# Kernel optimization log

Hardware: AMD Instinct MI355X
Metric: run time of the kernel (lower is better)

The kernel has to match this reference:

```python
import jax, jax.numpy as jnp
import numpy as np

N_NODES = 50000
IN_CH = 128
HID_CH = 128   # 2 * out_channels
OUT_CH = 64
N_EDGES = 800000


def setup_inputs() -> dict:
    key = jax.random.key(0)
    k1, k2, k3, k4 = jax.random.split(key, 4)
    x = jax.random.normal(k1, (N_NODES, IN_CH), dtype=jnp.float32)
    edge_index = jax.random.randint(k2, (2, N_EDGES), 0, N_NODES, dtype=jnp.int64)
    # Glorot-ish init for weights
    W1 = jax.random.normal(k3, (IN_CH, HID_CH), dtype=jnp.float32) * (1.0 / np.sqrt(IN_CH))
    b1 = jnp.zeros((HID_CH,), dtype=jnp.float32)
    W2 = jax.random.normal(k4, (HID_CH, OUT_CH), dtype=jnp.float32) * (1.0 / np.sqrt(HID_CH))
    b2 = jnp.zeros((OUT_CH,), dtype=jnp.float32)
    return {"x": x, "edge_index": edge_index, "W1": W1, "b1": b1, "W2": W2, "b2": b2}


def _gcn_norm(edge_index, num_nodes):
    """Add self-loops and compute symmetric normalization coeffs (PyG GCNConv default)."""
    loops = jnp.arange(num_nodes, dtype=edge_index.dtype)
    src = jnp.concatenate([edge_index[0], loops])  # [E + N]
    dst = jnp.concatenate([edge_index[1], loops])
    ones = jnp.ones_like(dst, dtype=jnp.float32)
    deg = jax.ops.segment_sum(ones, dst, num_segments=num_nodes)  # in-degree incl self-loop
    dinv = jnp.where(deg > 0, jax.lax.rsqrt(deg), 0.0)
    norm = dinv[src] * dinv[dst]  # [E + N]
    return src, dst, norm


def _gcn_conv(x, src, dst, norm, W, b, num_nodes):
    h = x @ W                                        # dense transform [N, d_out]
    msg = h[src] * norm[:, None]                     # gather + scale  [E+N, d_out]
    out = jax.ops.segment_sum(msg, dst, num_segments=num_nodes)  # scatter-add
    return out + b


def reference(x, edge_index, W1, b1, W2, b2):
    n = x.shape[0]
    src, dst, norm = _gcn_norm(edge_index, n)
    h = _gcn_conv(x, src, dst, norm, W1, b1, n)
    h = jax.nn.relu(h)
    out = _gcn_conv(h, src, dst, norm, W2, b2, n)
    return out
```

## Files before the change

### kernel.cpp

```cpp
#include <hip/hip_runtime.h>
#include <hip/hip_fp16.h>
#include <math.h>

#define IN_CH 128
#define CAP 64


__global__ __launch_bounds__(256, 4) void k_gemm_build(
    const float* __restrict__ x, const float* __restrict__ W1,
    __half* __restrict__ g1, int N,
    const int* __restrict__ src, const int* __restrict__ dst,
    int* __restrict__ deg, unsigned short* __restrict__ slot, int E, int GB) {
    constexpr int KC = 32;
    constexpr int AP = KC + 4;
    constexpr int NOUT = 128;
    constexpr int TCG = NOUT / 8;
    constexpr int BST = KC * 8 + 4;
    constexpr int TM = 4;
    __shared__ float As[64 * AP];
    __shared__ float Bs[TCG * BST];
    int tid = threadIdx.x;

    if ((int)blockIdx.x >= GB) {
        int base = ((int)blockIdx.x - GB) * 1024 + tid;
        int es[4], ed[4], er[4];
        bool ev[4];
#pragma unroll
        for (int k = 0; k < 4; ++k) {
            int e = base + k * 256;
            ev[k] = (e < E);
            ed[k] = ev[k] ? dst[e] : 0;
            es[k] = ev[k] ? src[e] : 0;
        }
#pragma unroll
        for (int k = 0; k < 4; ++k) er[k] = ev[k] ? atomicAdd(&deg[ed[k]], 1) : CAP;
#pragma unroll
        for (int k = 0; k < 4; ++k) {
            if (er[k] < CAP) slot[(size_t)ed[k] * CAP + er[k]] = (unsigned short)es[k];
        }
        return;
    }

    int row0 = (int)blockIdx.x * 64;
    int cg = tid % TCG;
    int rg = tid / TCG;
    int r0 = rg * TM;

    float acc[TM][8];
#pragma unroll
    for (int r = 0; r < TM; ++r)
#pragma unroll
        for (int c = 0; c < 8; ++c) acc[r][c] = 0.f;

    for (int kc0 = 0; kc0 < IN_CH; kc0 += KC) {
        if (kc0 > 0) __syncthreads();
        for (int idx = tid; idx < 64 * (KC / 4); idx += 256) {
            int r = idx >> 3;
            int c4 = (idx & 7) * 4;
            float4 v = make_float4(0.f, 0.f, 0.f, 0.f);
            if (row0 + r < N) v = *(const float4*)(x + (size_t)(row0 + r) * IN_CH + kc0 + c4);
            *(float4*)(As + r * AP + c4) = v;
        }
        for (int idx = tid; idx < KC * (NOUT / 4); idx += 256) {
            int kk = idx / (NOUT / 4);
            int col = (idx % (NOUT / 4)) * 4;
            int cgw = col >> 3;
            int j = col & 7;
            *(float4*)(Bs + cgw * BST + kk * 8 + j) = *(const float4*)(W1 + (size_t)(kc0 + kk) * NOUT + col);
        }
        __syncthreads();

        for (int k = 0; k < KC; k += 4) {
            float4 a4[TM];
#pragma unroll
            for (int r = 0; r < TM; ++r) a4[r] = *(const float4*)(As + (r0 + r) * AP + k);
#pragma unroll
            for (int kk = 0; kk < 4; ++kk) {
                float4 b0 = *(const float4*)(Bs + cg * BST + (k + kk) * 8);
                float4 b1 = *(const float4*)(Bs + cg * BST + (k + kk) * 8 + 4);
#pragma unroll
                for (int r = 0; r < TM; ++r) {
                    float a = (kk == 0) ? a4[r].x : (kk == 1) ? a4[r].y : (kk == 2) ? a4[r].z : a4[r].w;
                    acc[r][0] += a * b0.x;
                    acc[r][1] += a * b0.y;
                    acc[r][2] += a * b0.z;
                    acc[r][3] += a * b0.w;
                    acc[r][4] += a * b1.x;
                    acc[r][5] += a * b1.y;
                    acc[r][6] += a * b1.z;
                    acc[r][7] += a * b1.w;
                }
            }
        }
    }

#pragma unroll
    for (int r = 0; r < TM; ++r) {
        int row = row0 + r0 + r;
        if (row < N) {
            union { __half2 h[4]; uint4 u; } cv;
            cv.h[0] = __floats2half2_rn(acc[r][0], acc[r][1]);
            cv.h[1] = __floats2half2_rn(acc[r][2], acc[r][3]);
            cv.h[2] = __floats2half2_rn(acc[r][4], acc[r][5]);
            cv.h[3] = __floats2half2_rn(acc[r][6], acc[r][7]);
            *(uint4*)(g1 + (size_t)row * NOUT + cg * 8) = cv.u;
        }
    }
}

__global__ __launch_bounds__(256) void k_dinv(
    const int* __restrict__ deg, float* __restrict__ dinv, int N) {
    int i = blockIdx.x * 256 + threadIdx.x;
    if (i < N) dinv[i] = rsqrtf((float)(deg[i] + 1));
}


__global__ __launch_bounds__(256, 4) void k_gemm64(
    const __half* __restrict__ A, const float* __restrict__ W,
    const float* __restrict__ dinv, __half* __restrict__ G, int M) {
    constexpr int KC = 32;
    constexpr int AP = KC + 4;
    constexpr int NOUT = 64;
    constexpr int TCG = NOUT / 8;
    constexpr int BST = KC * 8 + 4;
    constexpr int TM = 2;
    __shared__ float As[64 * AP];
    __shared__ float Bs[TCG * BST];
    int tid = threadIdx.x;
    int row0 = blockIdx.x * 64;
    int cg = tid % TCG;
    int rg = tid / TCG;
    int r0 = rg * TM;

    float acc[TM][8];
#pragma unroll
    for (int r = 0; r < TM; ++r)
#pragma unroll
        for (int c = 0; c < 8; ++c) acc[r][c] = 0.f;

    for (int kc0 = 0; kc0 < IN_CH; kc0 += KC) {
        if (kc0 > 0) __syncthreads();
        {
            int r = tid >> 2;
            int grp = tid & 3;
            float f[8];
            if (row0 + r < M) {
                uint4 raw = *(const uint4*)(A + (size_t)(row0 + r) * IN_CH + kc0 + grp * 8);
                const __half2* h2 = (const __half2*)&raw;
#pragma unroll
                for (int q = 0; q < 4; ++q) {
                    float2 fv = __half22float2(h2[q]);
                    f[2 * q] = fv.x;
                    f[2 * q + 1] = fv.y;
                }
            } else {
#pragma unroll
                for (int q = 0; q < 8; ++q) f[q] = 0.f;
            }
            *(float4*)(As + r * AP + grp * 8) = make_float4(f[0], f[1], f[2], f[3]);
            *(float4*)(As + r * AP + grp * 8 + 4) = make_float4(f[4], f[5], f[6], f[7]);
        }
        for (int idx = tid; idx < KC * (NOUT / 4); idx += 256) {
            int kk = idx / (NOUT / 4);
            int col = (idx % (NOUT / 4)) * 4;
            int cgw = col >> 3;
            int j = col & 7;
            *(float4*)(Bs + cgw * BST + kk * 8 + j) = *(const float4*)(W + (size_t)(kc0 + kk) * NOUT + col);
        }
        __syncthreads();

        for (int k = 0; k < KC; k += 4) {
            float4 a4[TM];
#pragma unroll
            for (int r = 0; r < TM; ++r) a4[r] = *(const float4*)(As + (r0 + r) * AP + k);
#pragma unroll
            for (int kk = 0; kk < 4; ++kk) {
                float4 b0 = *(const float4*)(Bs + cg * BST + (k + kk) * 8);
                float4 b1 = *(const float4*)(Bs + cg * BST + (k + kk) * 8 + 4);
#pragma unroll
                for (int r = 0; r < TM; ++r) {
                    float a = (kk == 0) ? a4[r].x : (kk == 1) ? a4[r].y : (kk == 2) ? a4[r].z : a4[r].w;
                    acc[r][0] += a * b0.x;
                    acc[r][1] += a * b0.y;
                    acc[r][2] += a * b0.z;
                    acc[r][3] += a * b0.w;
                    acc[r][4] += a * b1.x;
                    acc[r][5] += a * b1.y;
                    acc[r][6] += a * b1.z;
                    acc[r][7] += a * b1.w;
                }
            }
        }
    }

#pragma unroll
    for (int r = 0; r < TM; ++r) {
        int row = row0 + r0 + r;
        if (row < M) {
            float d = dinv[row];
            union { __half2 h[4]; uint4 u; } cv;
            cv.h[0] = __floats2half2_rn(d * acc[r][0], d * acc[r][1]);
            cv.h[1] = __floats2half2_rn(d * acc[r][2], d * acc[r][3]);
            cv.h[2] = __floats2half2_rn(d * acc[r][4], d * acc[r][5]);
            cv.h[3] = __floats2half2_rn(d * acc[r][6], d * acc[r][7]);
            *(uint4*)(G + (size_t)row * NOUT + cg * 8) = cv.u;
        }
    }
}


__global__ __launch_bounds__(256) void k_agg128(
    const __half* __restrict__ g, const float* __restrict__ dinv,
    const unsigned short* __restrict__ slot,
    const float* __restrict__ bias, __half* __restrict__ out, int N,
    const int* __restrict__ deg) {
    int wave = threadIdx.x >> 6, lane = threadIdx.x & 63;
    int i = blockIdx.x * 4 + wave;
    if (i >= N) return;
    const __half2* gp = (const __half2*)g;
    int m = min(deg[i], CAP);
    float dinv_i = dinv[i];
    float2 self = __half22float2(gp[(size_t)i * 64 + lane]);
    float2 acc = make_float2(dinv_i * self.x, dinv_i * self.y);
    const unsigned short* sl = slot + (size_t)i * CAP;
    int r = 0;
    for (; r + 8 <= m; r += 8) {
        uint4 sraw = *(const uint4*)(sl + r);
        const unsigned short* sv = (const unsigned short*)&sraw;
        int s[8];
#pragma unroll
        for (int j = 0; j < 8; ++j) s[j] = sv[j];
        __half2 v[8];
#pragma unroll
        for (int j = 0; j < 8; ++j) v[j] = gp[(size_t)s[j] * 64 + lane];
        float ds[8];
#pragma unroll
        for (int j = 0; j < 8; ++j) ds[j] = dinv[s[j]];
#pragma unroll
        for (int j = 0; j < 8; ++j) {
            float2 f = __half22float2(v[j]);
            acc.x += ds[j] * f.x;
            acc.y += ds[j] * f.y;
        }
    }
    for (; r < m; ++r) {
        int s = sl[r];
        float dsv = dinv[s];
        float2 f = __half22float2(gp[(size_t)s * 64 + lane]);
        acc.x += dsv * f.x;
        acc.y += dsv * f.y;
    }
    float2 b = ((const float2*)bias)[lane];
    float ox = fmaxf(dinv_i * acc.x + b.x, 0.f);
    float oy = fmaxf(dinv_i * acc.y + b.y, 0.f);
    ((__half2*)out)[(size_t)i * 64 + lane] = __floats2half2_rn(ox, oy);
}

__global__ __launch_bounds__(256) void k_agg64(
    const __half* __restrict__ g, const float* __restrict__ dinv,
    const unsigned short* __restrict__ slot,
    const float* __restrict__ bias, float* __restrict__ out, int N,
    const int* __restrict__ deg) {
    int wave = threadIdx.x >> 6, lane = threadIdx.x & 63;
    int i = blockIdx.x * 4 + wave;
    if (i >= N) return;
    int m = min(deg[i], CAP);
    float dinv_i = dinv[i];
    float acc = __half2float(g[(size_t)i * 64 + lane]);
    const unsigned short* sl = slot + (size_t)i * CAP;
    int r = 0;
    for (; r + 8 <= m; r += 8) {
        uint4 sraw = *(const uint4*)(sl + r);
        const unsigned short* sv = (const unsigned short*)&sraw;
        int s[8];
#pragma unroll
        for (int j = 0; j < 8; ++j) s[j] = sv[j];
        __half v[8];
#pragma unroll
        for (int j = 0; j < 8; ++j) v[j] = g[(size_t)s[j] * 64 + lane];
#pragma unroll
        for (int j = 0; j < 8; ++j) acc += __half2float(v[j]);
    }
    for (; r < m; ++r) acc += __half2float(g[(size_t)sl[r] * 64 + lane]);
    out[(size_t)i * 64 + lane] = dinv_i * acc + bias[lane];
}


static inline size_t align256(size_t x) { return (x + 255) & ~(size_t)255; }

extern "C" void kernel_launch(void* const* d_in, const int* in_sizes, int n_in,
                              void* d_out, int out_size, void* d_ws, size_t ws_size,
                              hipStream_t stream) {
    const float* x = (const float*)d_in[0];
    const int* ei = (const int*)d_in[1];
    const float* W1 = (const float*)d_in[2];
    const float* b1 = (const float*)d_in[3];
    const float* W2 = (const float*)d_in[4];
    const float* b2 = (const float*)d_in[5];
    float* out = (float*)d_out;

    const int N = in_sizes[0] / IN_CH;
    const int E = in_sizes[1] / 2;
    const int* src = ei;
    const int* dst = ei + E;

    char* p = (char*)d_ws;
    int* deg = (int*)p;                 p += align256((size_t)N * 4);
    float* dinv = (float*)p;            p += align256((size_t)N * 4);
    unsigned short* slot = (unsigned short*)p;  p += align256((size_t)N * CAP * 2);
    __half* g1 = (__half*)p;            p += align256((size_t)N * 128 * 2);
    __half* a1 = (__half*)p;            p += align256((size_t)N * 128 * 2);
    __half* g2 = g1;

    const int GB = (N + 63) / 64;
    const int BB = (E + 1023) / 1024;

    hipMemsetAsync(deg, 0, (size_t)N * 4, stream);
    k_gemm_build<<<GB + BB, 256, 0, stream>>>(x, W1, g1, N, src, dst, deg, slot, E, GB);
    k_dinv<<<(N + 255) / 256, 256, 0, stream>>>(deg, dinv, N);
    k_agg128<<<(N + 3) / 4, 256, 0, stream>>>(g1, dinv, slot, b1, a1, N, deg);
    k_gemm64<<<GB, 256, 0, stream>>>(a1, W2, dinv, g2, N);
    k_agg64<<<(N + 3) / 4, 256, 0, stream>>>(g2, dinv, slot, b2, out, N, deg);
}
```

Baseline: 222.6 us.

## Fuse layer-1 aggregation into layer-2 GEMM via shared-memory tile

The first-layer neighbor aggregation (with bias and ReLU) is merged into the second-layer GEMM kernel. Each block aggregates its 64 rows into a float tile in shared memory, then multiplies that tile by W2. This removes the round trip of the fp16 a1 intermediate through global memory and one kernel launch, and adds a 16-wide unrolled gather loop. In exchange, only 782 blocks (4 waves each, 16 rows per wave, done in sequence) do the latency-bound gather, with more shared memory per block, so the memory parallelism available to hide gather latency may drop.

```diff
diff --git a/kernel.cpp b/kernel.cpp
--- a/kernel.cpp
+++ b/kernel.cpp
@@ -114,20 +114,91 @@
     if (i < N) dinv[i] = rsqrtf((float)(deg[i] + 1));
 }
 
-
-__global__ __launch_bounds__(256, 4) void k_gemm64(
-    const __half* __restrict__ A, const float* __restrict__ W,
-    const float* __restrict__ dinv, __half* __restrict__ G, int M) {
+__global__ __launch_bounds__(256, 3) void k_agg_gemm64(
+    const __half* __restrict__ g, const float* __restrict__ dinv,
+    const unsigned short* __restrict__ slot, const int* __restrict__ deg,
+    const float* __restrict__ b1, const float* __restrict__ W2,
+    __half* __restrict__ G, int N) {
+    constexpr int AFS = 132;
     constexpr int KC = 32;
-    constexpr int AP = KC + 4;
     constexpr int NOUT = 64;
     constexpr int TCG = NOUT / 8;
     constexpr int BST = KC * 8 + 4;
     constexpr int TM = 2;
-    __shared__ float As[64 * AP];
+    __shared__ float Af[64 * AFS];
     __shared__ float Bs[TCG * BST];
     int tid = threadIdx.x;
-    int row0 = blockIdx.x * 64;
+    int wave = tid >> 6, lane = tid & 63;
+    int row0 = (int)blockIdx.x * 64;
+    const __half2* gp = (const __half2*)g;
+
+    for (int t = 0; t < 16; ++t) {
+        int il = wave * 16 + t;
+        int i = row0 + il;
+        float2 acc = make_float2(0.f, 0.f);
+        if (i < N) {
+            int m = min(deg[i], CAP);
+            float di = dinv[i];
+            float2 self = __half22float2(gp[(size_t)i * 64 + lane]);
+            acc.x = di * self.x;
+            acc.y = di * self.y;
+            const unsigned short* sl = slot + (size_t)i * CAP;
+            int r = 0;
+            for (; r + 16 <= m; r += 16) {
+                uint4 sr0 = *(const uint4*)(sl + r);
+                uint4 sr1 = *(const uint4*)(sl + r + 8);
+                const unsigned short* sv0 = (const unsigned short*)&sr0;
+                const unsigned short* sv1 = (const unsigned short*)&sr1;
+                int s[16];
+#pragma unroll
+                for (int j = 0; j < 8; ++j) { s[j] = sv0[j]; s[8 + j] = sv1[j]; }
+                __half2 v[16];
+#pragma unroll
+                for (int j = 0; j < 16; ++j) v[j] = gp[(size_t)s[j] * 64 + lane];
+                float ds[16];
+#pragma unroll
+                for (int j = 0; j < 16; ++j) ds[j] = dinv[s[j]];
+#pragma unroll
+                for (int j = 0; j < 16; ++j) {
+                    float2 f = __half22float2(v[j]);
+                    acc.x += ds[j] * f.x;
+                    acc.y += ds[j] * f.y;
+                }
+            }
+            for (; r + 8 <= m; r += 8) {
+                uint4 sraw = *(const uint4*)(sl + r);
+                const unsigned short* sv = (const unsigned short*)&sraw;
+                int s[8];
+#pragma unroll
+                for (int j = 0; j < 8; ++j) s[j] = sv[j];
+                __half2 v[8];
+#pragma unroll
+                for (int j = 0; j < 8; ++j) v[j] = gp[(size_t)s[j] * 64 + lane];
+                float ds[8];
+#pragma unroll
+                for (int j = 0; j < 8; ++j) ds[j] = dinv[s[j]];
+#pragma unroll
+                for (int j = 0; j < 8; ++j) {
+                    float2 f = __half22float2(v[j]);
+                    acc.x += ds[j] * f.x;
+                    acc.y += ds[j] * f.y;
+                }
+            }
+            for (; r < m; ++r) {
+                int s = sl[r];
+                float dsv = dinv[s];
+                float2 f = __half22float2(gp[(size_t)s * 64 + lane]);
+                acc.x += dsv * f.x;
+                acc.y += dsv * f.y;
+            }
+            float2 b = ((const float2*)b1)[lane];
+            acc.x = fmaxf(di * acc.x + b.x, 0.f);
+            acc.y = fmaxf(di * acc.y + b.y, 0.f);
+        }
+        *(float2*)(Af + il * AFS + 2 * lane) = acc;
+    }
+    __syncthreads();
+
     int cg = tid % TCG;
     int rg = tid / TCG;
     int r0 = rg * TM;
@@ -140,43 +211,23 @@
 
     for (int kc0 = 0; kc0 < IN_CH; kc0 += KC) {
         if (kc0 > 0) __syncthreads();
-        {
-            int r = tid >> 2;
-            int grp = tid & 3;
-            float f[8];
-            if (row0 + r < M) {
-                uint4 raw = *(const uint4*)(A + (size_t)(row0 + r) * IN_CH + kc0 + grp * 8);
-                const __half2* h2 = (const __half2*)&raw;
-#pragma unroll
-                for (int q = 0; q < 4; ++q) {
-                    float2 fv = __half22float2(h2[q]);
-                    f[2 * q] = fv.x;
-                    f[2 * q + 1] = fv.y;
-                }
-            } else {
-#pragma unroll
-                for (int q = 0; q < 8; ++q) f[q] = 0.f;
-            }
-            *(float4*)(As + r * AP + grp * 8) = make_float4(f[0], f[1], f[2], f[3]);
-            *(float4*)(As + r * AP + grp * 8 + 4) = make_float4(f[4], f[5], f[6], f[7]);
-        }
         for (int idx = tid; idx < KC * (NOUT / 4); idx += 256) {
             int kk = idx / (NOUT / 4);
             int col = (idx % (NOUT / 4)) * 4;
             int cgw = col >> 3;
             int j = col & 7;
-            *(float4*)(Bs + cgw * BST + kk * 8 + j) = *(const float4*)(W + (size_t)(kc0 + kk) * NOUT + col);
+            *(float4*)(Bs + cgw * BST + kk * 8 + j) = *(const float4*)(W2 + (size_t)(kc0 + kk) * NOUT + col);
         }
         __syncthreads();
 
         for (int k = 0; k < KC; k += 4) {
             float4 a4[TM];
 #pragma unroll
-            for (int r = 0; r < TM; ++r) a4[r] = *(const float4*)(As + (r0 + r) * AP + k);
+            for (int r = 0; r < TM; ++r) a4[r] = *(const float4*)(Af + (r0 + r) * AFS + kc0 + k);
 #pragma unroll
             for (int kk = 0; kk < 4; ++kk) {
                 float4 b0 = *(const float4*)(Bs + cg * BST + (k + kk) * 8);
-                float4 b1 = *(const float4*)(Bs + cg * BST + (k + kk) * 8 + 4);
+                float4 b1v = *(const float4*)(Bs + cg * BST + (k + kk) * 8 + 4);
 #pragma unroll
                 for (int r = 0; r < TM; ++r) {
                     float a = (kk == 0) ? a4[r].x : (kk == 1) ? a4[r].y : (kk == 2) ? a4[r].z : a4[r].w;
@@ -184,10 +235,10 @@
                     acc[r][1] += a * b0.y;
                     acc[r][2] += a * b0.z;
                     acc[r][3] += a * b0.w;
-                    acc[r][4] += a * b1.x;
-                    acc[r][5] += a * b1.y;
-                    acc[r][6] += a * b1.z;
-                    acc[r][7] += a * b1.w;
+                    acc[r][4] += a * b1v.x;
+                    acc[r][5] += a * b1v.y;
+                    acc[r][6] += a * b1v.z;
+                    acc[r][7] += a * b1v.w;
                 }
             }
         }
@@ -196,7 +247,7 @@
 #pragma unroll
     for (int r = 0; r < TM; ++r) {
         int row = row0 + r0 + r;
-        if (row < M) {
+        if (row < N) {
             float d = dinv[row];
             union { __half2 h[4]; uint4 u; } cv;
             cv.h[0] = __floats2half2_rn(d * acc[r][0], d * acc[r][1]);
@@ -206,54 +257,6 @@
             *(uint4*)(G + (size_t)row * NOUT + cg * 8) = cv.u;
         }
     }
-}
-
-
-__global__ __launch_bounds__(256) void k_agg128(
-    const __half* __restrict__ g, const float* __restrict__ dinv,
-    const unsigned short* __restrict__ slot,
-    const float* __restrict__ bias, __half* __restrict__ out, int N,
-    const int* __restrict__ deg) {
-    int wave = threadIdx.x >> 6, lane = threadIdx.x & 63;
-    int i = blockIdx.x * 4 + wave;
-    if (i >= N) return;
-    const __half2* gp = (const __half2*)g;
-    int m = min(deg[i], CAP);
-    float dinv_i = dinv[i];
-    float2 self = __half22float2(gp[(size_t)i * 64 + lane]);
-    float2 acc = make_float2(dinv_i * self.x, dinv_i * self.y);
-    const unsigned short* sl = slot + (size_t)i * CAP;
-    int r = 0;
-    for (; r + 8 <= m; r += 8) {
-        uint4 sraw = *(const uint4*)(sl + r);
-        const unsigned short* sv = (const unsigned short*)&sraw;
-        int s[8];
-#pragma unroll
-        for (int j = 0; j < 8; ++j) s[j] = sv[j];
-        __half2 v[8];
-#pragma unroll
-        for (int j = 0; j < 8; ++j) v[j] = gp[(size_t)s[j] * 64 + lane];
-        float ds[8];
-#pragma unroll
-        for (int j = 0; j < 8; ++j) ds[j] = dinv[s[j]];
-#pragma unroll
-        for (int j = 0; j < 8; ++j) {
-            float2 f = __half22float2(v[j]);
-            acc.x += ds[j] * f.x;
-            acc.y += ds[j] * f.y;
-        }
-    }
-    for (; r < m; ++r) {
-        int s = sl[r];
-        float dsv = dinv[s];
-        float2 f = __half22float2(gp[(size_t)s * 64 + lane]);
-        acc.x += dsv * f.x;
-        acc.y += dsv * f.y;
-    }
-    float2 b = ((const float2*)bias)[lane];
-    float ox = fmaxf(dinv_i * acc.x + b.x, 0.f);
-    float oy = fmaxf(dinv_i * acc.y + b.y, 0.f);
-    ((__half2*)out)[(size_t)i * 64 + lane] = __floats2half2_rn(ox, oy);
 }
 
 __global__ __launch_bounds__(256) void k_agg64(
@@ -309,8 +312,7 @@
     float* dinv = (float*)p;            p += align256((size_t)N * 4);
     unsigned short* slot = (unsigned short*)p;  p += align256((size_t)N * CAP * 2);
     __half* g1 = (__half*)p;            p += align256((size_t)N * 128 * 2);
-    __half* a1 = (__half*)p;            p += align256((size_t)N * 128 * 2);
-    __half* g2 = g1;
+    __half* g2 = (__half*)p;            p += align256((size_t)N * 64 * 2);
 
     const int GB = (N + 63) / 64;
     const int BB = (E + 1023) / 1024;
@@ -318,7 +320,6 @@
     hipMemsetAsync(deg, 0, (size_t)N * 4, stream);
     k_gemm_build<<<GB + BB, 256, 0, stream>>>(x, W1, g1, N, src, dst, deg, slot, E, GB);
     k_dinv<<<(N + 255) / 256, 256, 0, stream>>>(deg, dinv, N);
-    k_agg128<<<(N + 3) / 4, 256, 0, stream>>>(g1, dinv, slot, b1, a1, N, deg);
-    k_gemm64<<<GB, 256, 0, stream>>>(a1, W2, dinv, g2, N);
+    k_agg_gemm64<<<GB, 256, 0, stream>>>(g1, dinv, slot, deg, b1, W2, g2, N);
     k_agg64<<<(N + 3) / 4, 256, 0, stream>>>(g2, dinv, slot, b2, out, N, deg);
 }
```

After: 288.9 us. 29.8% more time.
